# Performance work log

Hardware: AMD Instinct MI355X
Metric: run time of the kernel (lower is better)

Reference implementation:

```python
import jax, jax.numpy as jnp
import numpy as np

SHIFT = 1
EPS = 1e-5

def setup_inputs() -> dict:
    key = jax.random.key(0)
    k1, k2, k3, k4, k5, k6 = jax.random.split(key, 6)
    B, C, H, Wd = 64, 512, 28, 28
    Cout = 512
    return {
        "x": jax.random.normal(k1, (B, C, H, Wd), dtype=jnp.float32),
        "W": jax.random.normal(k2, (Cout, C), dtype=jnp.float32) * 0.05,
        "gamma": jax.random.uniform(k3, (Cout,), dtype=jnp.float32) + 0.5,
        "beta": jax.random.normal(k4, (Cout,), dtype=jnp.float32) * 0.1,
        "running_mean": jax.random.normal(k5, (Cout,), dtype=jnp.float32) * 0.1,
        "running_var": jax.random.uniform(k6, (Cout,), dtype=jnp.float32) + 0.5,
    }

def reference(x, W, gamma, beta, running_mean, running_var):
    # Group-wise spatial shift: split channels into 4 groups, roll each.
    Cg = x.shape[1] // 4
    x1 = jnp.roll(x[:, 0*Cg:1*Cg], -SHIFT, axis=2)  # up
    x2 = jnp.roll(x[:, 1*Cg:2*Cg],  SHIFT, axis=2)  # down
    x3 = jnp.roll(x[:, 2*Cg:3*Cg], -SHIFT, axis=3)  # left
    x4 = jnp.roll(x[:, 3*Cg:4*Cg],  SHIFT, axis=3)  # right
    shifted = jnp.concatenate([x1, x2, x3, x4], axis=1)  # [B,C,H,W]
    # 1x1 conv (no bias) == channel matmul
    y = jnp.einsum('bchw,oc->bohw', shifted, W)
    # BatchNorm (inference: running stats) folded to scale/shift, then ReLU
    scale = gamma * jax.lax.rsqrt(running_var + EPS)
    shift = beta - running_mean * scale
    y = y * scale[None, :, None, None] + shift[None, :, None, None]
    return jnp.maximum(y, 0.0)
```

## Files before the change

kernel.cpp:

```cpp
#include <hip/hip_runtime.h>

#define BN   64
#define CIN  512
#define COUT 512
#define HW   784
#define NT   128
#define MT   112
#define BK   64
#define NKB  (CIN / BK)
#define TROW 68

typedef __attribute__((ext_vector_type(8))) short short8;
typedef __attribute__((ext_vector_type(4))) float f32x4;

__device__ __forceinline__ unsigned short f2bf(float f) {
    union { float f; unsigned int u; } v; v.f = f;
    unsigned int r = v.u + 0x7fffu + ((v.u >> 16) & 1u);
    return (unsigned short)(r >> 16);
}

__device__ __forceinline__ uint2 pack4(float a, float b, float c, float d) {
    uint2 r;
    r.x = (unsigned int)f2bf(a) | ((unsigned int)f2bf(b) << 16);
    r.y = (unsigned int)f2bf(c) | ((unsigned int)f2bf(d) << 16);
    return r;
}

__device__ __forceinline__ void gl_lds16(const unsigned short* g, unsigned short* l) {
    __builtin_amdgcn_global_load_lds(
        (const __attribute__((address_space(1))) unsigned int*)g,
        (__attribute__((address_space(3))) unsigned int*)l,
        16, 0, 0);
}

__global__ __launch_bounds__(448)
void p1_shift_cvt(const float* __restrict__ x, const float* __restrict__ W,
                  unsigned short* __restrict__ Wb, unsigned short* __restrict__ Xt)
{
    __shared__ unsigned short sT[MT * TROW];
    const int t = threadIdx.x;
    if (blockIdx.z == BN) {
        int wlin = blockIdx.x * 7 + blockIdx.y;
        for (int gi = wlin * 448 + t; gi < (COUT * CIN) / 8; gi += 56 * 448) {
            const float* p = W + (size_t)gi * 8;
            float4 a = *(const float4*)p;
            float4 c = *(const float4*)(p + 4);
            uint2 lo = pack4(a.x, a.y, a.z, a.w);
            uint2 hi = pack4(c.x, c.y, c.z, c.w);
            uint4 v; v.x = lo.x; v.y = lo.y; v.z = hi.x; v.w = hi.y;
            *(uint4*)(Wb + (size_t)gi * 8) = v;
        }
        return;
    }
    const int kk = blockIdx.x;
    const int mt = blockIdx.y;
    const int b  = blockIdx.z;
    const int g  = kk >> 1;
    const int c0 = kk * BK;
    const int hw_base = mt * MT;
    const float* xb = x + (size_t)b * CIN * HW;

    {
        const int cq = t / 28;
        const int mq = t - cq * 28;
        const int hw = hw_base + mq * 4;
        const float* src = xb + (size_t)(c0 + cq * 4) * HW;
        float4 v0, v1, v2, v3;
        if (g < 2) {
            int shw = hw + (g == 0 ? 28 : HW - 28);
            if (shw >= HW) shw -= HW;
            v0 = *(const float4*)(src + 0 * HW + shw);
            v1 = *(const float4*)(src + 1 * HW + shw);
            v2 = *(const float4*)(src + 2 * HW + shw);
            v3 = *(const float4*)(src + 3 * HW + shw);
        } else {
            int h  = hw / 28;
            int w0 = hw - h * 28;
            int base = h * 28;
            #pragma unroll
            for (int j = 0; j < 4; ++j) {
                const float* row = src + j * HW + base;
                float4 a = *(const float4*)(row + w0);
                float4 r;
                if (g == 2) {
                    float ex = row[(w0 + 4 < 28) ? (w0 + 4) : 0];
                    r.x = a.y; r.y = a.z; r.z = a.w; r.w = ex;
                } else {
                    float ex = row[(w0 == 0) ? 27 : (w0 - 1)];
                    r.x = ex; r.y = a.x; r.z = a.y; r.w = a.z;
                }
                if (j == 0) v0 = r; else if (j == 1) v1 = r;
                else if (j == 2) v2 = r; else v3 = r;
            }
        }
        const int m0 = mq * 4;
        const int p  = (cq + mq) % 17;
        *(uint2*)(&sT[(m0 + 0) * TROW + p * 4]) = pack4(v0.x, v1.x, v2.x, v3.x);
        *(uint2*)(&sT[(m0 + 1) * TROW + p * 4]) = pack4(v0.y, v1.y, v2.y, v3.y);
        *(uint2*)(&sT[(m0 + 2) * TROW + p * 4]) = pack4(v0.z, v1.z, v2.z, v3.z);
        *(uint2*)(&sT[(m0 + 3) * TROW + p * 4]) = pack4(v0.w, v1.w, v2.w, v3.w);
    }
    __syncthreads();

    unsigned short* Xb = Xt + ((size_t)(b * 8 + kk) * HW + hw_base) * BK;
    #pragma unroll
    for (int e0 = 0; e0 < 2; ++e0) {
        int ch = t + e0 * 448;
        int m = ch >> 3, j = ch & 7;
        int q4 = m >> 2;
        int p0 = (2 * j + q4) % 17;
        int p1 = (2 * j + 1 + q4) % 17;
        uint2 a = *(const uint2*)(&sT[m * TROW + p0 * 4]);
        uint2 c = *(const uint2*)(&sT[m * TROW + p1 * 4]);
        uint4 v; v.x = a.x; v.y = a.y; v.z = c.x; v.w = c.y;
        *(uint4*)(Xb + (size_t)m * BK + j * 8) = v;
    }
}

__global__ __launch_bounds__(256, 2)
void p2_gemm(const unsigned short* __restrict__ Wb, const unsigned short* __restrict__ Xt,
             const float* __restrict__ gamma, const float* __restrict__ beta,
             const float* __restrict__ rmean, const float* __restrict__ rvar,
             float* __restrict__ out)
{
    __shared__ unsigned short sX[2][MT * BK];

    const int t  = threadIdx.x;
    const int id   = blockIdx.x;
    const int ot   = (id >> 3) & 1;
    const int pair = ((id >> 4) << 3) | (id & 7);
    const int mt   = pair % 7;
    const int b    = pair / 7;
    const int o_base  = ot * 256;
    const int hw_base = mt * MT;
    const int lane = t & 63;
    const int wv   = t >> 6;
    const int m16  = lane & 15;
    const int q    = lane >> 4;

    const unsigned short* Xbase = Xt + ((size_t)(b * 8) * HW + hw_base) * BK;

    auto stage = [&](int kk, int bufi) {
        unsigned short* buf = sX[bufi];
        const unsigned short* Xk = Xbase + (size_t)kk * HW * BK;
        int nci = (wv < 2) ? 4 : 3;
        for (int i = 0; i < nci; ++i) {
            int ci = wv + 4 * i;
            int ch = ci * 64 + lane;
            int hl = ch >> 3, sl = ch & 7;
            int cs = sl ^ (hl & 7);
            gl_lds16(Xk + hl * BK + cs * 8, &buf[ci * 512]);
        }
    };

    const unsigned short* wr0 = Wb + (size_t)(o_base + wv * 64 + m16) * CIN + q * 8;
    const unsigned short* wr1 = wr0 + 16 * CIN;
    const unsigned short* wr2 = wr0 + 32 * CIN;
    const unsigned short* wr3 = wr0 + 48 * CIN;

    f32x4 acc[4][7];
    #pragma unroll
    for (int i = 0; i < 4; ++i)
        #pragma unroll
        for (int j = 0; j < 7; ++j)
            acc[i][j] = (f32x4){0.f, 0.f, 0.f, 0.f};

    short8 wc[2][4], wn[2][4];
#define LOADW(DST, KK)                                  \
    {   const int ko = (KK) * 64;                       \
        DST[0][0] = *(const short8*)(wr0 + ko);         \
        DST[0][1] = *(const short8*)(wr1 + ko);         \
        DST[0][2] = *(const short8*)(wr2 + ko);         \
        DST[0][3] = *(const short8*)(wr3 + ko);         \
        DST[1][0] = *(const short8*)(wr0 + ko + 32);    \
        DST[1][1] = *(const short8*)(wr1 + ko + 32);    \
        DST[1][2] = *(const short8*)(wr2 + ko + 32);    \
        DST[1][3] = *(const short8*)(wr3 + ko + 32);    \
    }

#define MFMA16(A, B, C) __builtin_amdgcn_mfma_f32_16x16x32_bf16((A), (B), (C), 0, 0, 0)
#define COMPUTE(XS, WF)                                                          \
    {                                                                            \
        const unsigned short* xs = (XS);                                         \
        _Pragma("unroll")                                                        \
        for (int ks = 0; ks < 2; ++ks) {                                         \
            _Pragma("unroll")                                                    \
            for (int bm = 0; bm < 7; ++bm) {                                     \
                int m  = bm * 16 + m16;                                          \
                int lc = ks * 4 + q;                                             \
                int sl = lc ^ (m & 7);                                           \
                short8 bf = *(const short8*)(&xs[m * BK + sl * 8]);              \
                acc[0][bm] = MFMA16(WF[ks][0], bf, acc[0][bm]);                  \
                acc[1][bm] = MFMA16(WF[ks][1], bf, acc[1][bm]);                  \
                acc[2][bm] = MFMA16(WF[ks][2], bf, acc[2][bm]);                  \
                acc[3][bm] = MFMA16(WF[ks][3], bf, acc[3][bm]);                  \
            }                                                                    \
        }                                                                        \
    }

    stage(0, 0);
    LOADW(wc, 0);
    __syncthreads();

    #pragma unroll 1
    for (int kp = 0; kp < 4; ++kp) {
        {
            const int kn = 2 * kp + 1;
            stage(kn, 1);
            LOADW(wn, kn);
            COMPUTE(sX[0], wc);
            __syncthreads();
        }
        {
            const int kn = 2 * kp + 2;
            if (kn < NKB) {
                stage(kn, 0);
                LOADW(wc, kn);
            }
            COMPUTE(sX[1], wn);
            __syncthreads();
        }
    }
#undef COMPUTE
#undef MFMA16
#undef LOADW

    float scl[4][4], shf[4][4];
    #pragma unroll
    for (int bo = 0; bo < 4; ++bo)
        #pragma unroll
        for (int r = 0; r < 4; ++r) {
            int o = o_base + wv * 64 + bo * 16 + q * 4 + r;
            float sc = gamma[o] * rsqrtf(rvar[o] + 1e-5f);
            scl[bo][r] = sc;
            shf[bo][r] = beta[o] - rmean[o] * sc;
        }
    float* outb = out + (size_t)b * COUT * HW;
    #pragma unroll
    for (int bo = 0; bo < 4; ++bo) {
        #pragma unroll
        for (int r = 0; r < 4; ++r) {
            int o = o_base + wv * 64 + bo * 16 + q * 4 + r;
            float* orow = outb + (size_t)o * HW + hw_base + m16;
            #pragma unroll
            for (int bm = 0; bm < 7; ++bm) {
                float y = acc[bo][bm][r] * scl[bo][r] + shf[bo][r];
                y = fmaxf(y, 0.f);
                __builtin_nontemporal_store(y, orow + bm * 16);
            }
        }
    }
}

#define SW_STRIDE 72
#define SX_STRIDE 64
__global__ __launch_bounds__(256, 2)
void shiftconv_fallback(const float* __restrict__ x, const float* __restrict__ Wf,
                        const float* __restrict__ gamma, const float* __restrict__ beta,
                        const float* __restrict__ rmean, const float* __restrict__ rvar,
                        float* __restrict__ out)
{
    __shared__ unsigned short sW[NT * SW_STRIDE];
    __shared__ unsigned short sX[MT * SX_STRIDE];
    const int t = threadIdx.x;
    const int ot = blockIdx.x, mt = blockIdx.y, b = blockIdx.z;
    const int o_base = ot * NT, hw_base = mt * MT;
    const float* xb = x + (size_t)b * CIN * HW;
    const int lane = t & 63, wv = t >> 6, m16 = lane & 15, q = lane >> 4;
    f32x4 acc[2][7];
    #pragma unroll
    for (int i = 0; i < 2; ++i)
        #pragma unroll
        for (int j = 0; j < 7; ++j) acc[i][j] = (f32x4){0.f, 0.f, 0.f, 0.f};
    #pragma unroll
    for (int kk = 0; kk < CIN / BK; ++kk) {
        const int k0 = kk * BK;
        const int g = k0 >> 7;
        #pragma unroll
        for (int e0 = 0; e0 < 2; ++e0) {
            int e = t + e0 * 256;
            if (e < (BK / 4) * (MT / 4)) {
                int cq = e / 28, mq = e - cq * 28;
                int hw = hw_base + mq * 4;
                const float* src = xb + (size_t)(k0 + cq * 4) * HW;
                float4 v0, v1, v2, v3;
                if (g < 2) {
                    int shw = hw + (g == 0 ? 28 : HW - 28);
                    if (shw >= HW) shw -= HW;
                    v0 = *(const float4*)(src + 0 * HW + shw);
                    v1 = *(const float4*)(src + 1 * HW + shw);
                    v2 = *(const float4*)(src + 2 * HW + shw);
                    v3 = *(const float4*)(src + 3 * HW + shw);
                } else {
                    int h = hw / 28, w0 = hw - h * 28, base = h * 28;
                    #pragma unroll
                    for (int j = 0; j < 4; ++j) {
                        const float* row = src + j * HW + base;
                        float4 a = *(const float4*)(row + w0);
                        float4 r;
                        if (g == 2) {
                            float ex = row[(w0 + 4 < 28) ? (w0 + 4) : 0];
                            r.x = a.y; r.y = a.z; r.z = a.w; r.w = ex;
                        } else {
                            float ex = row[(w0 == 0) ? 27 : (w0 - 1)];
                            r.x = ex; r.y = a.x; r.z = a.y; r.w = a.z;
                        }
                        if (j == 0) v0 = r; else if (j == 1) v1 = r;
                        else if (j == 2) v2 = r; else v3 = r;
                    }
                }
                int m0 = mq * 4;
                { int p = (cq + 5 * (m0 + 0)) & 15;
                  *(uint2*)(&sX[(m0 + 0) * SX_STRIDE + p * 4]) = pack4(v0.x, v1.x, v2.x, v3.x); }
                { int p = (cq + 5 * (m0 + 1)) & 15;
                  *(uint2*)(&sX[(m0 + 1) * SX_STRIDE + p * 4]) = pack4(v0.y, v1.y, v2.y, v3.y); }
                { int p = (cq + 5 * (m0 + 2)) & 15;
                  *(uint2*)(&sX[(m0 + 2) * SX_STRIDE + p * 4]) = pack4(v0.z, v1.z, v2.z, v3.z); }
                { int p = (cq + 5 * (m0 + 3)) & 15;
                  *(uint2*)(&sX[(m0 + 3) * SX_STRIDE + p * 4]) = pack4(v0.w, v1.w, v2.w, v3.w); }
            }
        }
        #pragma unroll
        for (int i = 0; i < 4; ++i) {
            int e = t + i * 256;
            int ol = e >> 3, kg = (e & 7) * 8;
            const float* wr = Wf + (size_t)(o_base + ol) * CIN + k0 + kg;
            float4 a = *(const float4*)(wr);
            float4 c = *(const float4*)(wr + 4);
            uint2 lo = pack4(a.x, a.y, a.z, a.w);
            uint2 hi = pack4(c.x, c.y, c.z, c.w);
            uint4 v; v.x = lo.x; v.y = lo.y; v.z = hi.x; v.w = hi.y;
            *(uint4*)(&sW[ol * SW_STRIDE + kg]) = v;
        }
        __syncthreads();
        #pragma unroll
        for (int ks = 0; ks < BK; ks += 32) {
            short8 afrag[2];
            #pragma unroll
            for (int bo = 0; bo < 2; ++bo) {
                int row = wv * 32 + bo * 16 + m16;
                afrag[bo] = *(const short8*)(&sW[row * SW_STRIDE + ks + q * 8]);
            }
            #pragma unroll
            for (int bm = 0; bm < 7; ++bm) {
                int m = bm * 16 + m16;
                int g0 = (ks >> 2) + 2 * q;
                int p0 = (g0 + 5 * m) & 15;
                int p1 = (g0 + 1 + 5 * m) & 15;
                uint2 lo = *(const uint2*)(&sX[m * SX_STRIDE + p0 * 4]);
                uint2 hi = *(const uint2*)(&sX[m * SX_STRIDE + p1 * 4]);
                union { uint2 u2[2]; short8 s; } fb;
                fb.u2[0] = lo; fb.u2[1] = hi;
                acc[0][bm] = __builtin_amdgcn_mfma_f32_16x16x32_bf16(afrag[0], fb.s, acc[0][bm], 0, 0, 0);
                acc[1][bm] = __builtin_amdgcn_mfma_f32_16x16x32_bf16(afrag[1], fb.s, acc[1][bm], 0, 0, 0);
            }
        }
        __syncthreads();
    }
    float scl[2][4], shf[2][4];
    #pragma unroll
    for (int bo = 0; bo < 2; ++bo)
        #pragma unroll
        for (int r = 0; r < 4; ++r) {
            int o = o_base + wv * 32 + bo * 16 + q * 4 + r;
            float sc = gamma[o] * rsqrtf(rvar[o] + 1e-5f);
            scl[bo][r] = sc;
            shf[bo][r] = beta[o] - rmean[o] * sc;
        }
    float* outb = out + (size_t)b * COUT * HW;
    #pragma unroll
    for (int bo = 0; bo < 2; ++bo)
        #pragma unroll
        for (int r = 0; r < 4; ++r) {
            int o = o_base + wv * 32 + bo * 16 + q * 4 + r;
            float* orow = outb + (size_t)o * HW + hw_base + m16;
            #pragma unroll
            for (int bm = 0; bm < 7; ++bm) {
                float y = acc[bo][bm][r] * scl[bo][r] + shf[bo][r];
                y = fmaxf(y, 0.f);
                __builtin_nontemporal_store(y, orow + bm * 16);
            }
        }
}

extern "C" void kernel_launch(void* const* d_in, const int* in_sizes, int n_in,
                              void* d_out, int out_size, void* d_ws, size_t ws_size,
                              hipStream_t stream)
{
    const float* x     = (const float*)d_in[0];
    const float* W     = (const float*)d_in[1];
    const float* gamma = (const float*)d_in[2];
    const float* beta  = (const float*)d_in[3];
    const float* rmean = (const float*)d_in[4];
    const float* rvar  = (const float*)d_in[5];
    float* out = (float*)d_out;

    const size_t wb_bytes = (size_t)COUT * CIN * 2;
    const size_t xt_bytes = (size_t)BN * CIN * HW * 2;
    if (ws_size >= wb_bytes + xt_bytes) {
        unsigned short* Wb = (unsigned short*)d_ws;
        unsigned short* Xt = (unsigned short*)((char*)d_ws + wb_bytes);
        dim3 g1(8, 7, BN + 1);
        p1_shift_cvt<<<g1, 448, 0, stream>>>(x, W, Wb, Xt);
        p2_gemm<<<896, 256, 0, stream>>>(Wb, Xt, gamma, beta, rmean, rvar, out);
    } else {
        dim3 grid(COUT / NT, HW / MT, BN);
        shiftconv_fallback<<<grid, 256, 0, stream>>>(x, W, gamma, beta, rmean, rvar, out);
    }
}
```

Measured before the change: 232.2 us.

## Deepen LDS pipeline to four buffers with prefetch distance two and partial vmcnt waits

The X tiles in shared memory go from double to quadruple buffering, and each tile is staged two k-steps ahead. The k-loop is fully unrolled into explicit phases. Each full __syncthreads is replaced by a barrier that waits only on the older outstanding global loads, using per-wave vmcnt counts. The aim is to hide global-to-LDS latency behind MFMA work, at the cost of doubling LDS use per block (about 57KB), which may hurt the two-blocks-per-CU occupancy target, and of relying on exact hand-counted vmcnt values.

```diff
diff --git a/kernel.cpp b/kernel.cpp
--- a/kernel.cpp
+++ b/kernel.cpp
@@ -123,7 +123,7 @@
              const float* __restrict__ rmean, const float* __restrict__ rvar,
              float* __restrict__ out)
 {
-    __shared__ unsigned short sX[2][MT * BK];
+    __shared__ unsigned short sX[4][MT * BK];
 
     const int t  = threadIdx.x;
     const int id   = blockIdx.x;
@@ -143,7 +143,7 @@
     auto stage = [&](int kk, int bufi) {
         unsigned short* buf = sX[bufi];
         const unsigned short* Xk = Xbase + (size_t)kk * HW * BK;
-        int nci = (wv < 2) ? 4 : 3;
+        const int nci = (wv < 2) ? 4 : 3;
         for (int i = 0; i < nci; ++i) {
             int ci = wv + 4 * i;
             int ch = ci * 64 + lane;
@@ -198,29 +198,37 @@
         }                                                                        \
     }
 
+#define BARC(K12, K11)                                                           \
+    {   __builtin_amdgcn_sched_barrier(0);                                       \
+        if (wv < 2) asm volatile("s_waitcnt vmcnt(" #K12 ")" ::: "memory");      \
+        else        asm volatile("s_waitcnt vmcnt(" #K11 ")" ::: "memory");      \
+        __builtin_amdgcn_s_barrier();                                            \
+        __builtin_amdgcn_sched_barrier(0);                                       \
+    }
+
     stage(0, 0);
     LOADW(wc, 0);
-    __syncthreads();
-
-    #pragma unroll 1
-    for (int kp = 0; kp < 4; ++kp) {
-        {
-            const int kn = 2 * kp + 1;
-            stage(kn, 1);
-            LOADW(wn, kn);
-            COMPUTE(sX[0], wc);
-            __syncthreads();
-        }
-        {
-            const int kn = 2 * kp + 2;
-            if (kn < NKB) {
-                stage(kn, 0);
-                LOADW(wc, kn);
-            }
-            COMPUTE(sX[1], wn);
-            __syncthreads();
-        }
-    }
+    stage(1, 1);
+    BARC(12, 11);
+
+#define PHASE(K, WCUR, WNXT)                    \
+    LOADW(WNXT, (K) + 1);                       \
+    stage((K) + 2, ((K) + 2) & 3);              \
+    COMPUTE(sX[(K) & 3], WCUR);                 \
+    BARC(12, 11);
+
+    PHASE(0, wc, wn)
+    PHASE(1, wn, wc)
+    PHASE(2, wc, wn)
+    PHASE(3, wn, wc)
+    PHASE(4, wc, wn)
+    PHASE(5, wn, wc)
+    LOADW(wn, 7);
+    COMPUTE(sX[2], wc);
+    BARC(8, 8);
+    COMPUTE(sX[3], wn);
+#undef PHASE
+#undef BARC
 #undef COMPUTE
 #undef MFMA16
 #undef LOADW
```

Result: no change. 230.0 us (-0.9%).
